# Kernel optimization log

Measured on AMD Instinct MI355X. Metric: run time of the kernel, lower is better.

Reference implementation:

```python
import jax, jax.numpy as jnp
import numpy as np

STRIDE, PADDING, EPS = 2, 1, 1e-5


def setup_inputs() -> dict:
    key = jax.random.key(0)
    k1, k2, k3 = jax.random.split(key, 3)
    C_in, C_out, K = 64, 64, 4
    x = jax.random.normal(k1, (32, C_in, 64, 64), dtype=jnp.float32)
    weight = jax.random.normal(k2, (C_in, C_out, K, K), dtype=jnp.float32) * 0.05  # torch layout (in,out,kh,kw)
    conv_bias = jax.random.normal(k3, (C_out,), dtype=jnp.float32) * 0.02
    gamma = jnp.ones((C_out,), dtype=jnp.float32)
    beta = jnp.zeros((C_out,), dtype=jnp.float32)
    running_mean = jnp.zeros((C_out,), dtype=jnp.float32)
    running_var = jnp.ones((C_out,), dtype=jnp.float32)
    return {"x": x, "weight": weight, "conv_bias": conv_bias, "gamma": gamma,
            "beta": beta, "running_mean": running_mean, "running_var": running_var}


def _conv_transpose2d(x, weight, bias, stride, padding):
    # torch.nn.functional.conv_transpose2d equivalent:
    # conv with lhs_dilation=stride, spatially-flipped kernel, in/out axes swapped,
    # and padding k-1-p on each side.
    k = weight.shape[2]
    w_t = jnp.transpose(jnp.flip(weight, (2, 3)), (1, 0, 2, 3))  # (Cout, Cin, k, k)
    pad = k - 1 - padding
    y = jax.lax.conv_general_dilated(
        x, w_t,
        window_strides=(1, 1),
        padding=[(pad, pad), (pad, pad)],
        lhs_dilation=(stride, stride),
        dimension_numbers=("NCHW", "OIHW", "NCHW"),
    )
    return y + bias[None, :, None, None]


def reference(x, weight, conv_bias, gamma, beta, running_mean, running_var):
    # ConvTranspose2d
    y = _conv_transpose2d(x, weight, conv_bias, STRIDE, PADDING)  # [N,C,128,128]
    # BatchNorm2d (inference, running stats)
    scale = gamma * jax.lax.rsqrt(running_var + EPS)
    y = (y - running_mean[None, :, None, None]) * scale[None, :, None, None] + beta[None, :, None, None]
    # Softmax over channel dim
    y = jax.nn.softmax(y, axis=1)
    # MaxPool2d(k=2, s=2): H,W are even, so reshape-max is exact
    N, C, H, W = y.shape
    y = y.reshape(N, C, H // 2, 2, W // 2, 2).max(axis=(3, 5))  # [N,C,64,64]
    return y
```

## Files before the change

kernel.cpp:

```cpp
#include <hip/hip_runtime.h>
#include <math.h>


typedef __attribute__((ext_vector_type(8))) short short8;
typedef __attribute__((ext_vector_type(4))) float floatx4;

#define COLS 66

__device__ ushort g_wfrag[4 * 8 * 4 * 64 * 8];
__device__ float g_aff[128];

__device__ __forceinline__ ushort f2bf(float f) {
  union { float f; unsigned u; } v; v.f = f;
  unsigned r = v.u + 0x7FFF + ((v.u >> 16) & 1);
  return (ushort)(r >> 16);
}

__global__ __launch_bounds__(256) void prep_kernel(
    const float* __restrict__ w, const float* __restrict__ bias,
    const float* __restrict__ gamma, const float* __restrict__ beta,
    const float* __restrict__ mean, const float* __restrict__ var) {
  int t = blockIdx.x * 256 + threadIdx.x;
  int cin0 = (t >> 6) * 8;
  int cout = t & 63;
  int pack[16][4];
#pragma unroll
  for (int e = 0; e < 16; ++e)
#pragma unroll
    for (int i = 0; i < 4; ++i) pack[e][i] = 0;

  for (int ci = 0; ci < 8; ++ci) {
    const float4* p = (const float4*)&w[((cin0 + ci) * 64 + cout) * 16];
    float4 f0 = p[0], f1 = p[1], f2 = p[2], f3 = p[3];
    float f[16] = {f0.x, f0.y, f0.z, f0.w, f1.x, f1.y, f1.z, f1.w,
                   f2.x, f2.y, f2.z, f2.w, f3.x, f3.y, f3.z, f3.w};
#pragma unroll
    for (int e = 0; e < 16; ++e)
      pack[e][ci >> 1] |= ((int)f2bf(f[e])) << ((ci & 1) * 16);
  }

  int ksq = cin0 >> 5;
  int q   = (cin0 >> 3) & 3;
  int nt = cout >> 4, b15 = cout & 15;
#pragma unroll
  for (int kh = 0; kh < 4; ++kh)
#pragma unroll
    for (int kw = 0; kw < 4; ++kw) {
      int r = (kh & 1) ? 0 : 1;
      int pp = (kw & 1) ? 0 : 1;
      int c = r * 2 + pp;
      int tap = (kh >> 1) * 2 + (kw >> 1);
      int ks = tap * 2 + ksq;
      int4 pk = {pack[kh * 4 + kw][0], pack[kh * 4 + kw][1],
                 pack[kh * 4 + kw][2], pack[kh * 4 + kw][3]};
      *(int4*)&g_wfrag[((((c * 8 + ks) * 4 + nt) * 64) + q * 16 + b15) * 8] = pk;
    }

  if (t < 64) {
    float A = gamma[t] * rsqrtf(var[t] + 1e-5f);
    g_aff[t] = A;
    g_aff[64 + t] = (bias[t] - mean[t]) * A + beta[t];
  }
}

__global__ __launch_bounds__(256, 3) void fused_kernel(const float* __restrict__ x,
                                                       float* __restrict__ out) {
  __shared__ ushort xs[4 * COLS * 64];
  __shared__ ushort wbuf[16 * 512];

  const int tid  = threadIdx.x;
  const int ph0  = blockIdx.x * 2;
  const int n    = blockIdx.y;
  const int wave = tid >> 6;
  const int lane = tid & 63;
  const int b15  = lane & 15;
  const int q    = lane >> 4;
  const int wr   = wave >> 1;
  const int wc   = wave & 1;

  for (int e = tid; e < 4 * 16 * 32; e += 256) {
    int iw2 = e & 31;
    int c4  = (e >> 5) & 15;
    int row = e >> 9;
    int ih  = ph0 - 1 + row;
    float2 v0 = {0.f, 0.f}, v1 = v0, v2 = v0, v3 = v0;
    if (ih >= 0 && ih < 64) {
      const float* xp = x + ((n * 64 + c4 * 4) * 64 + ih) * 64 + iw2 * 2;
      v0 = *(const float2*)xp;          v1 = *(const float2*)(xp + 4096);
      v2 = *(const float2*)(xp + 8192); v3 = *(const float2*)(xp + 12288);
    }
    int chunk = c4 >> 1, half4 = (c4 & 1) * 4;
    {
      int col = iw2 * 2 + 1;
      ushort4 pk; pk.x = f2bf(v0.x); pk.y = f2bf(v1.x); pk.z = f2bf(v2.x); pk.w = f2bf(v3.x);
      *(ushort4*)&xs[(row * COLS + col) * 64 + ((chunk ^ (col & 7)) * 8) + half4] = pk;
    }
    {
      int col = iw2 * 2 + 2;
      ushort4 pk; pk.x = f2bf(v0.y); pk.y = f2bf(v1.y); pk.z = f2bf(v2.y); pk.w = f2bf(v3.y);
      *(ushort4*)&xs[(row * COLS + col) * 64 + ((chunk ^ (col & 7)) * 8) + half4] = pk;
    }
  }
  for (int e = tid; e < 4 * 2 * 16; e += 256) {
    int c4 = e & 15, side = (e >> 4) & 1, row = e >> 5;
    int col = side ? 65 : 0;
    int chunk = c4 >> 1, half4 = (c4 & 1) * 4;
    ushort4 z; z.x = z.y = z.z = z.w = 0;
    *(ushort4*)&xs[(row * COLS + col) * 64 + ((chunk ^ (col & 7)) * 8) + half4] = z;
  }
  __syncthreads();

  float Ac[4], Dc[4];
#pragma unroll
  for (int nt = 0; nt < 4; ++nt) {
    Ac[nt] = g_aff[nt * 16 + b15];
    Dc[nt] = g_aff[64 + nt * 16 + b15];
  }

  floatx4 pooled[8];
#pragma unroll
  for (int i = 0; i < 8; ++i) pooled[i] = (floatx4){0.f, 0.f, 0.f, 0.f};

  for (int c = 0; c < 4; ++c) {
    const int r = c >> 1, p = c & 1;
    floatx4 acc[8];
#pragma unroll
    for (int i = 0; i < 8; ++i) acc[i] = (floatx4){0.f, 0.f, 0.f, 0.f};

    for (int h = 0; h < 2; ++h) {
#pragma unroll
      for (int ff = 0; ff < 4; ++ff) {
        int f = wave * 4 + ff;
        int ks_l = f >> 2, nt = f & 3;
        int gf = (c * 8 + h * 4 + ks_l) * 4 + nt;
        const ushort* gsrc = &g_wfrag[gf * 512 + lane * 8];
        __builtin_amdgcn_global_load_lds(
            (const __attribute__((address_space(1))) void*)gsrc,
            (__attribute__((address_space(3))) void*)&wbuf[f * 512], 16, 0, 0);
      }
      __syncthreads();

#pragma unroll
      for (int ks_l = 0; ks_l < 4; ++ks_l) {
        const int ks = h * 4 + ks_l;
        const int tap = ks >> 1, a = tap >> 1, b = tap & 1;
        const int hrow = wr + (r ? (a ? 1 : 2) : (a ? 0 : 1));
        const int dx   = p ? (b ? 0 : 1) : (b ? -1 : 0);
        const int chunk = (ks & 1) * 4 + q;
        short8 af[2];
#pragma unroll
        for (int mt = 0; mt < 2; ++mt) {
          int col = wc * 32 + mt * 16 + b15 + dx + 1;
          af[mt] = *(const short8*)&xs[(hrow * COLS + col) * 64 + ((chunk ^ (col & 7)) * 8)];
        }
#pragma unroll
        for (int nt = 0; nt < 4; ++nt) {
          short8 bf = *(const short8*)&wbuf[(ks_l * 4 + nt) * 512 + lane * 8];
#pragma unroll
          for (int mt = 0; mt < 2; ++mt)
            acc[mt * 4 + nt] =
                __builtin_amdgcn_mfma_f32_16x16x32_bf16(af[mt], bf, acc[mt * 4 + nt], 0, 0, 0);
        }
      }
      __syncthreads();
    }

#pragma unroll
    for (int mt = 0; mt < 2; ++mt) {
      float v[16];
      float sm[4] = {0.f, 0.f, 0.f, 0.f};
#pragma unroll
      for (int nt = 0; nt < 4; ++nt)
#pragma unroll
        for (int reg = 0; reg < 4; ++reg) {
          float e = __expf(fmaf(acc[mt * 4 + nt][reg], Ac[nt], Dc[nt]));
          v[nt * 4 + reg] = e;
          sm[reg] += e;
        }
#pragma unroll
      for (int reg = 0; reg < 4; ++reg) {
        sm[reg] += __shfl_xor(sm[reg], 1, 64);
        sm[reg] += __shfl_xor(sm[reg], 2, 64);
        sm[reg] += __shfl_xor(sm[reg], 4, 64);
        sm[reg] += __shfl_xor(sm[reg], 8, 64);
        sm[reg] = 1.0f / sm[reg];
      }
#pragma unroll
      for (int nt = 0; nt < 4; ++nt)
#pragma unroll
        for (int reg = 0; reg < 4; ++reg)
          pooled[mt * 4 + nt][reg] =
              fmaxf(pooled[mt * 4 + nt][reg], v[nt * 4 + reg] * sm[reg]);
    }
  }

  float* red = (float*)xs;
#pragma unroll
  for (int mt = 0; mt < 2; ++mt)
#pragma unroll
    for (int nt = 0; nt < 4; ++nt)
#pragma unroll
      for (int reg = 0; reg < 4; ++reg)
        red[(wr * 64 + nt * 16 + b15) * 66 + wc * 32 + mt * 16 + q * 4 + reg] =
            pooled[mt * 4 + nt][reg];
  __syncthreads();
  for (int e = tid; e < 4096; e += 256) {
    int pw2  = e & 31;
    int cout = (e >> 5) & 63;
    int rl   = e >> 11;
    float2 val = *(float2*)&red[(rl * 64 + cout) * 66 + pw2 * 2];
    *(float2*)&out[((n * 64 + cout) * 64 + (ph0 + rl)) * 64 + pw2 * 2] = val;
  }
}

extern "C" void kernel_launch(void* const* d_in, const int* in_sizes, int n_in,
                              void* d_out, int out_size, void* d_ws, size_t ws_size,
                              hipStream_t stream) {
  const float* x     = (const float*)d_in[0];
  const float* w     = (const float*)d_in[1];
  const float* bias  = (const float*)d_in[2];
  const float* gamma = (const float*)d_in[3];
  const float* beta  = (const float*)d_in[4];
  const float* mean  = (const float*)d_in[5];
  const float* var   = (const float*)d_in[6];
  float* out = (float*)d_out;

  prep_kernel<<<2, 256, 0, stream>>>(w, bias, gamma, beta, mean, var);
  dim3 grid(32, 32);
  fused_kernel<<<grid, 256, 0, stream>>>(x, out);
}
```

Before: 127.3 us.

## Load weight fragments directly from global, drop LDS weight staging and syncs

The main kernel now reads packed bf16 weight fragments straight from global memory (L2/L1-resident) into registers instead of staging them through an LDS buffer with barriers. This removes 16 KB of LDS per block and two barriers per half-step, and occupancy is raised to 4 blocks per SM. The prep kernel is reparallelized over 8 blocks, each thread packing two input channels. The cost is more global or cache traffic per wave and exposed load latency before the MFMAs.

```diff
diff --git a/kernel.cpp b/kernel.cpp
--- a/kernel.cpp
+++ b/kernel.cpp
@@ -21,27 +21,24 @@
     const float* __restrict__ gamma, const float* __restrict__ beta,
     const float* __restrict__ mean, const float* __restrict__ var) {
   int t = blockIdx.x * 256 + threadIdx.x;
-  int cin0 = (t >> 6) * 8;
+  int cin0 = (t >> 6) * 2;
   int cout = t & 63;
-  int pack[16][4];
-#pragma unroll
-  for (int e = 0; e < 16; ++e)
-#pragma unroll
-    for (int i = 0; i < 4; ++i) pack[e][i] = 0;
-
-  for (int ci = 0; ci < 8; ++ci) {
-    const float4* p = (const float4*)&w[((cin0 + ci) * 64 + cout) * 16];
-    float4 f0 = p[0], f1 = p[1], f2 = p[2], f3 = p[3];
-    float f[16] = {f0.x, f0.y, f0.z, f0.w, f1.x, f1.y, f1.z, f1.w,
-                   f2.x, f2.y, f2.z, f2.w, f3.x, f3.y, f3.z, f3.w};
-#pragma unroll
-    for (int e = 0; e < 16; ++e)
-      pack[e][ci >> 1] |= ((int)f2bf(f[e])) << ((ci & 1) * 16);
-  }
-
+  int nt = cout >> 4, b15 = cout & 15;
+  int q = (cin0 & 31) >> 3;
+  int j = cin0 & 7;
   int ksq = cin0 >> 5;
-  int q   = (cin0 >> 3) & 3;
-  int nt = cout >> 4, b15 = cout & 15;
+
+  const float4* p0 = (const float4*)&w[(cin0 * 64 + cout) * 16];
+  const float4* p1 = (const float4*)&w[((cin0 + 1) * 64 + cout) * 16];
+  float a[16], b[16];
+  {
+    float4 f0 = p0[0], f1 = p0[1], f2 = p0[2], f3 = p0[3];
+    a[0]=f0.x; a[1]=f0.y; a[2]=f0.z; a[3]=f0.w; a[4]=f1.x; a[5]=f1.y; a[6]=f1.z; a[7]=f1.w;
+    a[8]=f2.x; a[9]=f2.y; a[10]=f2.z; a[11]=f2.w; a[12]=f3.x; a[13]=f3.y; a[14]=f3.z; a[15]=f3.w;
+    float4 g0 = p1[0], g1 = p1[1], g2 = p1[2], g3 = p1[3];
+    b[0]=g0.x; b[1]=g0.y; b[2]=g0.z; b[3]=g0.w; b[4]=g1.x; b[5]=g1.y; b[6]=g1.z; b[7]=g1.w;
+    b[8]=g2.x; b[9]=g2.y; b[10]=g2.z; b[11]=g2.w; b[12]=g3.x; b[13]=g3.y; b[14]=g3.z; b[15]=g3.w;
+  }
 #pragma unroll
   for (int kh = 0; kh < 4; ++kh)
 #pragma unroll
@@ -51,9 +48,8 @@
       int c = r * 2 + pp;
       int tap = (kh >> 1) * 2 + (kw >> 1);
       int ks = tap * 2 + ksq;
-      int4 pk = {pack[kh * 4 + kw][0], pack[kh * 4 + kw][1],
-                 pack[kh * 4 + kw][2], pack[kh * 4 + kw][3]};
-      *(int4*)&g_wfrag[((((c * 8 + ks) * 4 + nt) * 64) + q * 16 + b15) * 8] = pk;
+      unsigned u = (unsigned)f2bf(a[kh * 4 + kw]) | ((unsigned)f2bf(b[kh * 4 + kw]) << 16);
+      *(unsigned*)&g_wfrag[(((c * 8 + ks) * 4 + nt) * 64 + q * 16 + b15) * 8 + j] = u;
     }
 
   if (t < 64) {
@@ -63,10 +59,9 @@
   }
 }
 
-__global__ __launch_bounds__(256, 3) void fused_kernel(const float* __restrict__ x,
+__global__ __launch_bounds__(256, 4) void fused_kernel(const float* __restrict__ x,
                                                        float* __restrict__ out) {
   __shared__ ushort xs[4 * COLS * 64];
-  __shared__ ushort wbuf[16 * 512];
 
   const int tid  = threadIdx.x;
   const int ph0  = blockIdx.x * 2;
@@ -127,42 +122,28 @@
 #pragma unroll
     for (int i = 0; i < 8; ++i) acc[i] = (floatx4){0.f, 0.f, 0.f, 0.f};
 
-    for (int h = 0; h < 2; ++h) {
-#pragma unroll
-      for (int ff = 0; ff < 4; ++ff) {
-        int f = wave * 4 + ff;
-        int ks_l = f >> 2, nt = f & 3;
-        int gf = (c * 8 + h * 4 + ks_l) * 4 + nt;
-        const ushort* gsrc = &g_wfrag[gf * 512 + lane * 8];
-        __builtin_amdgcn_global_load_lds(
-            (const __attribute__((address_space(1))) void*)gsrc,
-            (__attribute__((address_space(3))) void*)&wbuf[f * 512], 16, 0, 0);
+#pragma unroll
+    for (int ks = 0; ks < 8; ++ks) {
+      const int tap = ks >> 1, a = tap >> 1, b = tap & 1;
+      const int hrow = wr + (r ? (a ? 1 : 2) : (a ? 0 : 1));
+      const int dx   = p ? (b ? 0 : 1) : (b ? -1 : 0);
+      const int chunk = (ks & 1) * 4 + q;
+      const short8* wf = (const short8*)&g_wfrag[((c * 8 + ks) * 4) * 512];
+      short8 bf[4];
+#pragma unroll
+      for (int nt = 0; nt < 4; ++nt) bf[nt] = wf[nt * 64 + lane];
+      short8 af[2];
+#pragma unroll
+      for (int mt = 0; mt < 2; ++mt) {
+        int col = wc * 32 + mt * 16 + b15 + dx + 1;
+        af[mt] = *(const short8*)&xs[(hrow * COLS + col) * 64 + ((chunk ^ (col & 7)) * 8)];
       }
-      __syncthreads();
-
-#pragma unroll
-      for (int ks_l = 0; ks_l < 4; ++ks_l) {
-        const int ks = h * 4 + ks_l;
-        const int tap = ks >> 1, a = tap >> 1, b = tap & 1;
-        const int hrow = wr + (r ? (a ? 1 : 2) : (a ? 0 : 1));
-        const int dx   = p ? (b ? 0 : 1) : (b ? -1 : 0);
-        const int chunk = (ks & 1) * 4 + q;
-        short8 af[2];
-#pragma unroll
-        for (int mt = 0; mt < 2; ++mt) {
-          int col = wc * 32 + mt * 16 + b15 + dx + 1;
-          af[mt] = *(const short8*)&xs[(hrow * COLS + col) * 64 + ((chunk ^ (col & 7)) * 8)];
-        }
-#pragma unroll
-        for (int nt = 0; nt < 4; ++nt) {
-          short8 bf = *(const short8*)&wbuf[(ks_l * 4 + nt) * 512 + lane * 8];
-#pragma unroll
-          for (int mt = 0; mt < 2; ++mt)
-            acc[mt * 4 + nt] =
-                __builtin_amdgcn_mfma_f32_16x16x32_bf16(af[mt], bf, acc[mt * 4 + nt], 0, 0, 0);
-        }
-      }
-      __syncthreads();
+#pragma unroll
+      for (int nt = 0; nt < 4; ++nt)
+#pragma unroll
+        for (int mt = 0; mt < 2; ++mt)
+          acc[mt * 4 + nt] =
+              __builtin_amdgcn_mfma_f32_16x16x32_bf16(af[mt], bf[nt], acc[mt * 4 + nt], 0, 0, 0);
     }
 
 #pragma unroll
@@ -194,6 +175,7 @@
     }
   }
 
+  __syncthreads();
   float* red = (float*)xs;
 #pragma unroll
   for (int mt = 0; mt < 2; ++mt)
@@ -225,7 +207,7 @@
   const float* var   = (const float*)d_in[6];
   float* out = (float*)d_out;
 
-  prep_kernel<<<2, 256, 0, stream>>>(w, bias, gamma, beta, mean, var);
+  prep_kernel<<<8, 256, 0, stream>>>(w, bias, gamma, beta, mean, var);
   dim3 grid(32, 32);
   fused_kernel<<<grid, 256, 0, stream>>>(x, out);
 }
```

Measured after the change: 122.1 us. 4.0% less time.
